# Kernel tuning notes

Hardware: AMD Instinct MI355X
Metric: run time of the kernel (lower is better)

## Reference

```python
import jax, jax.numpy as jnp
import numpy as np

N_ATOM, N_BOND, N_MOL, D = 250000, 250000, 10000, 64
BN_EPS = 1e-5


def _bn(x, gamma, beta):
    # torch BatchNorm1d training-mode math (biased variance)
    m = jnp.mean(x, axis=0)
    v = jnp.var(x, axis=0)
    return (x - m) * jax.lax.rsqrt(v + BN_EPS) * gamma + beta


def setup_inputs() -> dict:
    key = jax.random.key(0)
    ks = jax.random.split(key, 12)
    h = jax.random.normal(ks[0], (N_ATOM, D), jnp.float32)
    e = jax.random.normal(ks[1], (N_BOND, D), jnp.float32)
    u = jax.random.normal(ks[2], (N_MOL, D), jnp.float32)
    norm_atom = jax.random.uniform(ks[3], (N_ATOM, 1), jnp.float32)
    norm_bond = jax.random.uniform(ks[4], (N_BOND, 1), jnp.float32)
    bond_u = jax.random.randint(ks[5], (N_BOND,), 0, N_ATOM, jnp.int32)
    bond_v = jax.random.randint(ks[6], (N_BOND,), 0, N_ATOM, jnp.int32)
    atom2mol = jax.random.randint(ks[7], (N_ATOM,), 0, N_MOL, jnp.int32)
    bond2mol = jax.random.randint(ks[8], (N_BOND,), 0, N_MOL, jnp.int32)
    # 9 Linear layers A..I stacked: order A,B,C,D,E,F,G,H,I
    Ws = jax.random.normal(ks[9], (9, D, D), jnp.float32) * 0.05
    bs = jax.random.normal(ks[10], (9, D), jnp.float32) * 0.05
    bn_gamma = jnp.ones((3, D), jnp.float32)   # [e, h, u]
    bn_beta = jnp.zeros((3, D), jnp.float32)
    return dict(h=h, e=e, u=u, norm_atom=norm_atom, norm_bond=norm_bond,
                Ws=Ws, bs=bs, bn_gamma=bn_gamma, bn_beta=bn_beta,
                bond_u=bond_u, bond_v=bond_v, atom2mol=atom2mol, bond2mol=bond2mol)


def reference(h, e, u, norm_atom, norm_bond, Ws, bs, bn_gamma, bn_beta,
              bond_u, bond_v, atom2mol, bond2mol):
    lin = lambda x, i: x @ Ws[i] + bs[i]
    Ah, Dh, Eh = lin(h, 0), lin(h, 3), lin(h, 4)
    Be = lin(e, 1)
    Cu, Fu = lin(u, 2), lin(u, 5)

    # bond update: a2b (sum of Ah of both endpoints) + b2b self-loop + g2b broadcast
    e_new = Ah[bond_u] + Ah[bond_v] + Be + Cu[bond2mol]
    e_new = e_new * norm_bond                  # graph_norm
    e_new = _bn(e_new, bn_gamma[0], bn_beta[0])
    e_new = jax.nn.elu(e_new)

    # atom update: a2a self-loop + gated b2a (select_not_equal == other endpoint's Eh) + g2a
    sig = jax.nn.sigmoid(e_new)                # [N_BOND, D]
    dst = jnp.concatenate([bond_u, bond_v])    # each bond sends to both endpoints
    Eh_other = jnp.concatenate([Eh[bond_v], Eh[bond_u]])
    sig2 = jnp.concatenate([sig, sig])
    num = jax.ops.segment_sum(sig2 * Eh_other, dst, num_segments=N_ATOM)
    den = jax.ops.segment_sum(sig2, dst, num_segments=N_ATOM) + 1e-6
    h_new = Dh + num / den + Fu[atom2mol]
    h_new = h_new * norm_atom                  # graph_norm
    h_new = _bn(h_new, bn_gamma[1], bn_beta[1])
    h_new = jax.nn.elu(h_new)

    # global update: mean(Gh over atoms) + mean(He over bonds) + g2g self-loop Iu
    Gh, He, Iu = lin(h_new, 6), lin(e_new, 7), lin(u, 8)
    cnt_a = jax.ops.segment_sum(jnp.ones((N_ATOM, 1), h.dtype), atom2mol, num_segments=N_MOL)
    cnt_b = jax.ops.segment_sum(jnp.ones((N_BOND, 1), e.dtype), bond2mol, num_segments=N_MOL)
    u_new = (jax.ops.segment_sum(Gh, atom2mol, num_segments=N_MOL) / jnp.maximum(cnt_a, 1.0)
             + jax.ops.segment_sum(He, bond2mol, num_segments=N_MOL) / jnp.maximum(cnt_b, 1.0)
             + Iu)
    u_new = _bn(u_new, bn_gamma[2], bn_beta[2])
    u_new = jax.nn.elu(u_new)

    return h_new, e_new, u_new
```

## Files before the change

kernel.cpp:

```cpp
#include <hip/hip_runtime.h>
#include <cmath>

#define DD 64
#define TILE 64
#define BLK 256
#define NSLOT 64

__device__ __forceinline__ float elu_f(float x) {
  return x > 0.f ? x : expm1f(x);
}
__device__ __forceinline__ float sigmoid_fast(float x) {
  return __builtin_amdgcn_rcpf(1.f + __expf(-x));
}

__device__ __forceinline__ void fma4(float4& a, float s, const float4 b) {
  a.x = fmaf(s, b.x, a.x);
  a.y = fmaf(s, b.y, a.y);
  a.z = fmaf(s, b.z, a.z);
  a.w = fmaf(s, b.w, a.w);
}
__device__ __forceinline__ void add4(float4& a, const float4 b) {
  a.x += b.x; a.y += b.y; a.z += b.z; a.w += b.w;
}
__device__ __forceinline__ void sqacc4(float4& a, const float4 b) {
  a.x = fmaf(b.x, b.x, a.x);
  a.y = fmaf(b.y, b.y, a.y);
  a.z = fmaf(b.z, b.z, a.z);
  a.w = fmaf(b.w, b.w, a.w);
}
__device__ __forceinline__ void scale4(float4& a, float s) {
  a.x *= s; a.y *= s; a.z *= s; a.w *= s;
}

__device__ __forceinline__ void matmul_tile(const float (*xs)[DD + 4], const float (*wl)[DD],
                                            int r0, int c0, float4 acc[4]) {
#pragma unroll 2
  for (int k0 = 0; k0 < DD; k0 += 4) {
    float4 x0 = *(const float4*)&xs[r0 + 0][k0];
    float4 x1 = *(const float4*)&xs[r0 + 1][k0];
    float4 x2 = *(const float4*)&xs[r0 + 2][k0];
    float4 x3 = *(const float4*)&xs[r0 + 3][k0];
    float4 w0 = *(const float4*)&wl[k0 + 0][c0];
    float4 w1 = *(const float4*)&wl[k0 + 1][c0];
    float4 w2 = *(const float4*)&wl[k0 + 2][c0];
    float4 w3 = *(const float4*)&wl[k0 + 3][c0];
    fma4(acc[0], x0.x, w0); fma4(acc[0], x0.y, w1); fma4(acc[0], x0.z, w2); fma4(acc[0], x0.w, w3);
    fma4(acc[1], x1.x, w0); fma4(acc[1], x1.y, w1); fma4(acc[1], x1.z, w2); fma4(acc[1], x1.w, w3);
    fma4(acc[2], x2.x, w0); fma4(acc[2], x2.y, w1); fma4(acc[2], x2.z, w2); fma4(acc[2], x2.w, w3);
    fma4(acc[3], x3.x, w0); fma4(acc[3], x3.y, w1); fma4(acc[3], x3.z, w2); fma4(acc[3], x3.w, w3);
  }
}

__global__ void cnt_kernel(const int* __restrict__ a2m, int na,
                           const int* __restrict__ b2m, int nb,
                           const int* __restrict__ bu, const int* __restrict__ bv,
                           int* __restrict__ cnta_i, int* __restrict__ cntb_i,
                           int* __restrict__ deg) {
  int i = blockIdx.x * blockDim.x + threadIdx.x;
  if (i < na) {
    atomicAdd(&cnta_i[a2m[i]], 1);
  } else if (i < na + nb) {
    int b = i - na;
    atomicAdd(&cntb_i[b2m[b]], 1);
    atomicAdd(&deg[bu[b]], 1);
    atomicAdd(&deg[bv[b]], 1);
  }
}

__global__ void seg_alloc_kernel(const int* __restrict__ deg, int n,
                                 int* __restrict__ start, int* __restrict__ gcount) {
  int i = blockIdx.x * blockDim.x + threadIdx.x;
  int lane = threadIdx.x & 63;
  int d = (i < n) ? deg[i] : 0;
  int pre = d;
#pragma unroll
  for (int off = 1; off < 64; off <<= 1) {
    int t = __shfl_up(pre, off, 64);
    if (lane >= off) pre += t;
  }
  int total = __shfl(pre, 63, 64);
  int excl = pre - d;
  int base = 0;
  if (lane == 63) base = atomicAdd(gcount, total);
  base = __shfl(base, 63, 64);
  if (i < n) start[i] = base + excl;
}

__global__ void fill_kernel(const int* __restrict__ bu, const int* __restrict__ bv, int nb,
                            const int* __restrict__ start, int* __restrict__ cur,
                            int2* __restrict__ adj) {
  int b = blockIdx.x * blockDim.x + threadIdx.x;
  if (b < nb) {
    int a0 = bu[b], a1 = bv[b];
    int p = start[a0] + atomicAdd(&cur[a0], 1);
    adj[p] = make_int2(b, a1);
    int q = start[a1] + atomicAdd(&cur[a1], 1);
    adj[q] = make_int2(b, a0);
  }
}

__global__ void fill_mol_kernel(const int* __restrict__ a2m, int na,
                                const int* __restrict__ b2m, int nb,
                                const int* __restrict__ start_ma, int* __restrict__ cur_ma,
                                int* __restrict__ lista,
                                const int* __restrict__ start_mb, int* __restrict__ cur_mb,
                                int* __restrict__ listb) {
  int i = blockIdx.x * blockDim.x + threadIdx.x;
  if (i < na) {
    int m = a2m[i];
    lista[start_ma[m] + atomicAdd(&cur_ma[m], 1)] = i;
  } else if (i < na + nb) {
    int b = i - na;
    int m = b2m[b];
    listb[start_mb[m] + atomicAdd(&cur_mb[m], 1)] = b;
  }
}

__global__ __launch_bounds__(BLK) void lin2_kernel(
    const float* __restrict__ x, int nrows,
    const float* __restrict__ W0, const float* __restrict__ b0, float* __restrict__ out0,
    const float* __restrict__ W1, const float* __restrict__ b1, float* __restrict__ out1) {
  __shared__ __align__(16) float xs[TILE][DD + 4];
  __shared__ __align__(16) float w0[DD][DD];
  __shared__ __align__(16) float w1[DD][DD];
  const int tid = threadIdx.x;
  const int base = blockIdx.x * TILE;
  int rows = nrows - base; if (rows > TILE) rows = TILE;
  for (int l = tid; l < DD * DD; l += BLK) {
    int r = l >> 6, c = l & 63;
    xs[r][c] = (r < rows) ? x[(size_t)(base + r) * DD + c] : 0.f;
    w0[r][c] = W0[l];
    w1[r][c] = W1[l];
  }
  __syncthreads();
  const int tr = tid >> 4, tc = tid & 15;
  const int r0 = tr * 4, c0 = tc * 4;
  float4 accA[4], accB[4];
#pragma unroll
  for (int i = 0; i < 4; ++i) {
    accA[i] = make_float4(0.f, 0.f, 0.f, 0.f);
    accB[i] = make_float4(0.f, 0.f, 0.f, 0.f);
  }
#pragma unroll 1
  for (int k0 = 0; k0 < DD; k0 += 4) {
    float4 x0 = *(const float4*)&xs[r0 + 0][k0];
    float4 x1 = *(const float4*)&xs[r0 + 1][k0];
    float4 x2 = *(const float4*)&xs[r0 + 2][k0];
    float4 x3 = *(const float4*)&xs[r0 + 3][k0];
    float4 wa0 = *(const float4*)&w0[k0 + 0][c0];
    float4 wa1 = *(const float4*)&w0[k0 + 1][c0];
    float4 wa2 = *(const float4*)&w0[k0 + 2][c0];
    float4 wa3 = *(const float4*)&w0[k0 + 3][c0];
    float4 wb0 = *(const float4*)&w1[k0 + 0][c0];
    float4 wb1 = *(const float4*)&w1[k0 + 1][c0];
    float4 wb2 = *(const float4*)&w1[k0 + 2][c0];
    float4 wb3 = *(const float4*)&w1[k0 + 3][c0];
    fma4(accA[0], x0.x, wa0); fma4(accA[0], x0.y, wa1); fma4(accA[0], x0.z, wa2); fma4(accA[0], x0.w, wa3);
    fma4(accA[1], x1.x, wa0); fma4(accA[1], x1.y, wa1); fma4(accA[1], x1.z, wa2); fma4(accA[1], x1.w, wa3);
    fma4(accA[2], x2.x, wa0); fma4(accA[2], x2.y, wa1); fma4(accA[2], x2.z, wa2); fma4(accA[2], x2.w, wa3);
    fma4(accA[3], x3.x, wa0); fma4(accA[3], x3.y, wa1); fma4(accA[3], x3.z, wa2); fma4(accA[3], x3.w, wa3);
    fma4(accB[0], x0.x, wb0); fma4(accB[0], x0.y, wb1); fma4(accB[0], x0.z, wb2); fma4(accB[0], x0.w, wb3);
    fma4(accB[1], x1.x, wb0); fma4(accB[1], x1.y, wb1); fma4(accB[1], x1.z, wb2); fma4(accB[1], x1.w, wb3);
    fma4(accB[2], x2.x, wb0); fma4(accB[2], x2.y, wb1); fma4(accB[2], x2.z, wb2); fma4(accB[2], x2.w, wb3);
    fma4(accB[3], x3.x, wb0); fma4(accB[3], x3.y, wb1); fma4(accB[3], x3.z, wb2); fma4(accB[3], x3.w, wb3);
  }
  float4 bv0 = *(const float4*)&b0[c0];
  float4 bv1 = *(const float4*)&b1[c0];
#pragma unroll
  for (int i = 0; i < 4; ++i) {
    if (r0 + i < rows) {
      size_t rb = (size_t)(base + r0 + i) * DD + c0;
      float4 o0 = accA[i]; add4(o0, bv0);
      float4 o1 = accB[i]; add4(o1, bv1);
      *(float4*)&out0[rb] = o0;
      *(float4*)&out1[rb] = o1;
    }
  }
}

__global__ __launch_bounds__(BLK) void lin1_kernel(
    const float* __restrict__ x, int nrows,
    const float* __restrict__ W, const float* __restrict__ b, float* __restrict__ out) {
  __shared__ __align__(16) float xs[TILE][DD + 4];
  __shared__ __align__(16) float wl[DD][DD];
  const int tid = threadIdx.x;
  const int base = blockIdx.x * TILE;
  int rows = nrows - base; if (rows > TILE) rows = TILE;
  for (int l = tid; l < DD * DD; l += BLK) {
    int r = l >> 6, c = l & 63;
    xs[r][c] = (r < rows) ? x[(size_t)(base + r) * DD + c] : 0.f;
    wl[r][c] = W[l];
  }
  __syncthreads();
  const int tr = tid >> 4, tc = tid & 15;
  const int r0 = tr * 4, c0 = tc * 4;
  float4 acc[4];
#pragma unroll
  for (int i = 0; i < 4; ++i) acc[i] = make_float4(0.f, 0.f, 0.f, 0.f);
  matmul_tile(xs, wl, r0, c0, acc);
  float4 bv = *(const float4*)&b[c0];
#pragma unroll
  for (int i = 0; i < 4; ++i) {
    if (r0 + i < rows) {
      size_t rb = (size_t)(base + r0 + i) * DD + c0;
      float4 o = acc[i]; add4(o, bv);
      *(float4*)&out[rb] = o;
    }
  }
}

__global__ __launch_bounds__(BLK) void bond1_kernel(
    const float* __restrict__ e, int nrows, int ntiles,
    const float* __restrict__ W1, const float* __restrict__ b1,
    const float* __restrict__ Ah, const float* __restrict__ Cu,
    const int* __restrict__ bu, const int* __restrict__ bv, const int* __restrict__ b2m,
    const float* __restrict__ nrm,
    float* __restrict__ e_pre,
    float* __restrict__ psum, float* __restrict__ psq) {
  __shared__ __align__(16) float xs[TILE][DD + 4];
  __shared__ __align__(16) float wl[DD][DD];
  __shared__ int sbu[TILE], sbv[TILE], sbm[TILE];
  __shared__ float snb[TILE];
  __shared__ __align__(16) float red[16][DD];
  const int tid = threadIdx.x;
  const int tr = tid >> 4, tc = tid & 15, r0 = tr * 4, c0 = tc * 4;
  for (int l = tid; l < DD * DD; l += BLK) wl[l >> 6][l & 63] = W1[l];
  float4 bp = *(const float4*)&b1[c0];
  float4 lsum = make_float4(0.f, 0.f, 0.f, 0.f);
  float4 lsq  = make_float4(0.f, 0.f, 0.f, 0.f);
  for (int tile = blockIdx.x; tile < ntiles; tile += gridDim.x) {
    const int base = tile * TILE;
    int rows = nrows - base; if (rows > TILE) rows = TILE;
    __syncthreads();
    for (int l = tid; l < TILE * DD; l += BLK) {
      int r = l >> 6, c = l & 63;
      xs[r][c] = (r < rows) ? e[(size_t)(base + r) * DD + c] : 0.f;
    }
    if (tid < TILE) {
      bool v = tid < rows;
      int rb = base + tid;
      sbu[tid] = v ? bu[rb] : 0;
      sbv[tid] = v ? bv[rb] : 0;
      sbm[tid] = v ? b2m[rb] : 0;
      snb[tid] = v ? nrm[rb] : 0.f;
    }
    __syncthreads();
    float4 acc[4];
#pragma unroll
    for (int i = 0; i < 4; ++i) acc[i] = make_float4(0.f, 0.f, 0.f, 0.f);
    matmul_tile(xs, wl, r0, c0, acc);
#pragma unroll
    for (int i = 0; i < 4; ++i) {
      int r = r0 + i;
      if (r < rows) {
        int rb = base + r;
        float nb = snb[r];
        float4 ga = *(const float4*)&Ah[(size_t)sbu[r] * DD + c0];
        float4 gb = *(const float4*)&Ah[(size_t)sbv[r] * DD + c0];
        float4 gc = *(const float4*)&Cu[(size_t)sbm[r] * DD + c0];
        float4 o = acc[i];
        add4(o, bp); add4(o, ga); add4(o, gb); add4(o, gc);
        scale4(o, nb);
        add4(lsum, o); sqacc4(lsq, o);
        *(float4*)&e_pre[(size_t)rb * DD + c0] = o;
      }
    }
  }
  __syncthreads();
  *(float4*)&red[tr][c0] = lsum;
  __syncthreads();
  const int slot = (blockIdx.x & (NSLOT - 1)) * DD;
  if (tid < DD) {
    float s = 0.f;
#pragma unroll
    for (int t = 0; t < 16; ++t) s += red[t][tid];
    atomicAdd(&psum[slot + tid], s);
  }
  __syncthreads();
  *(float4*)&red[tr][c0] = lsq;
  __syncthreads();
  if (tid < DD) {
    float s = 0.f;
#pragma unroll
    for (int t = 0; t < 16; ++t) s += red[t][tid];
    atomicAdd(&psq[slot + tid], s);
  }
}

__global__ void bnfinal_kernel(const float* __restrict__ ssum, const float* __restrict__ ssq,
                               const float* __restrict__ gamma, const float* __restrict__ beta,
                               float invN, float* __restrict__ scale, float* __restrict__ shift) {
  int j = threadIdx.x;
  float m = ssum[j] * invN;
  float v = ssq[j] * invN - m * m;
  float sc = gamma[j] * rsqrtf(v + 1e-5f);
  scale[j] = sc;
  shift[j] = beta[j] - m * sc;
}

__global__ void bnfinal_slots_kernel(const float* __restrict__ psum, const float* __restrict__ psq,
                                     const float* __restrict__ gamma, const float* __restrict__ beta,
                                     float invN, float* __restrict__ scale, float* __restrict__ shift) {
  int j = threadIdx.x;
  float s = 0.f, q = 0.f;
#pragma unroll 8
  for (int t = 0; t < NSLOT; ++t) {
    s += psum[t * DD + j];
    q += psq[t * DD + j];
  }
  float m = s * invN;
  float v = q * invN - m * m;
  float sc = gamma[j] * rsqrtf(v + 1e-5f);
  scale[j] = sc;
  shift[j] = beta[j] - m * sc;
}

__global__ void bn_elu_vec_kernel(float* __restrict__ x, long n4,
                                  const float* __restrict__ scale,
                                  const float* __restrict__ shift) {
  long stride = (long)gridDim.x * blockDim.x;
  for (long i = blockIdx.x * (long)blockDim.x + threadIdx.x; i < n4; i += stride) {
    float4 v = ((float4*)x)[i];
    int c0 = (int)((i & 15) << 2);
    float4 sc = *(const float4*)&scale[c0];
    float4 sh = *(const float4*)&shift[c0];
    v.x = elu_f(fmaf(v.x, sc.x, sh.x));
    v.y = elu_f(fmaf(v.y, sc.y, sh.y));
    v.z = elu_f(fmaf(v.z, sc.z, sh.z));
    v.w = elu_f(fmaf(v.w, sc.w, sh.w));
    ((float4*)x)[i] = v;
  }
}

__global__ __launch_bounds__(BLK) void agg_fused_kernel(
    const float* __restrict__ e_act, const float* __restrict__ Eh,
    const float* __restrict__ Dhb, const float* __restrict__ Fu,
    const int* __restrict__ a2m, const float* __restrict__ nrm,
    const int* __restrict__ start, const int* __restrict__ deg,
    const int2* __restrict__ adj, int na,
    float* __restrict__ hpre,
    float* __restrict__ psum, float* __restrict__ psq) {
  const int tid = threadIdx.x;
  const int lane = tid & 63;
  const int wv = tid >> 6;
  const int wid = blockIdx.x * (BLK >> 6) + wv;
  float lsum = 0.f, lsq = 0.f;
  if (wid < na) {
    float dh = Dhb[(size_t)wid * DD + lane];
    float fu = Fu[(size_t)a2m[wid] * DD + lane];
    float nr = nrm[wid];
    int s = start[wid], d = deg[wid];
    float num = 0.f, den = 0.f;
    int k = 0;
    for (; k + 2 <= d; k += 2) {
      int2 e0 = adj[s + k];
      int2 e1 = adj[s + k + 1];
      float ev0 = e_act[(size_t)e0.x * DD + lane];
      float eh0 = Eh[(size_t)e0.y * DD + lane];
      float ev1 = e_act[(size_t)e1.x * DD + lane];
      float eh1 = Eh[(size_t)e1.y * DD + lane];
      float sg0 = sigmoid_fast(ev0);
      float sg1 = sigmoid_fast(ev1);
      num = fmaf(sg0, eh0, num); den += sg0;
      num = fmaf(sg1, eh1, num); den += sg1;
    }
    if (k < d) {
      int2 e0 = adj[s + k];
      float ev = e_act[(size_t)e0.x * DD + lane];
      float eh = Eh[(size_t)e0.y * DD + lane];
      float sg = sigmoid_fast(ev);
      num = fmaf(sg, eh, num); den += sg;
    }
    float o = (dh + num / (den + 1e-6f) + fu) * nr;
    hpre[(size_t)wid * DD + lane] = o;
    lsum = o;
    lsq = o * o;
  }
  __shared__ __align__(16) float red[BLK / 64][DD];
  red[wv][lane] = lsum;
  __syncthreads();
  if (tid < DD) {
    float s4 = red[0][tid] + red[1][tid] + red[2][tid] + red[3][tid];
    atomicAdd(&psum[(blockIdx.x & (NSLOT - 1)) * DD + tid], s4);
  }
  __syncthreads();
  red[wv][lane] = lsq;
  __syncthreads();
  if (tid < DD) {
    float s4 = red[0][tid] + red[1][tid] + red[2][tid] + red[3][tid];
    atomicAdd(&psq[(blockIdx.x & (NSLOT - 1)) * DD + tid], s4);
  }
}

__global__ __launch_bounds__(BLK) void molsum2_kernel(
    const float* __restrict__ srcA, const int* __restrict__ start_ma,
    const int* __restrict__ cnta, const int* __restrict__ lista,
    const float* __restrict__ srcB, const int* __restrict__ start_mb,
    const int* __restrict__ cntb, const int* __restrict__ listb,
    int nm, float* __restrict__ msa, float* __restrict__ msb) {
  int wid = (int)((blockIdx.x * (unsigned)blockDim.x + threadIdx.x) >> 6);
  int lane = threadIdx.x & 63;
  if (wid >= 2 * nm) return;
  const float* src;
  const int* list;
  float* out;
  int m, s, c;
  if (wid < nm) {
    m = wid; src = srcA; list = lista; out = msa;
    s = start_ma[m]; c = cnta[m];
  } else {
    m = wid - nm; src = srcB; list = listb; out = msb;
    s = start_mb[m]; c = cntb[m];
  }
  float acc = 0.f;
  int k = 0;
  for (; k + 2 <= c; k += 2) {
    int i0 = list[s + k], i1 = list[s + k + 1];
    float v0 = src[(size_t)i0 * DD + lane];
    float v1 = src[(size_t)i1 * DD + lane];
    acc += v0 + v1;
  }
  if (k < c) acc += src[(size_t)list[s + k] * DD + lane];
  out[(size_t)m * DD + lane] = acc;
}

__global__ __launch_bounds__(BLK) void global1_kernel(
    const float* __restrict__ u, int nrows,
    const float* __restrict__ W6, const float* __restrict__ W7, const float* __restrict__ W8,
    const float* __restrict__ b6, const float* __restrict__ b7, const float* __restrict__ b8,
    const float* __restrict__ msa, const float* __restrict__ msb,
    const int* __restrict__ cnta, const int* __restrict__ cntb,
    float* __restrict__ upre,
    float* __restrict__ ssum, float* __restrict__ ssq) {
  __shared__ __align__(16) float xsu[TILE][DD + 4];
  __shared__ __align__(16) float xsa[TILE][DD + 4];
  __shared__ __align__(16) float xsb[TILE][DD + 4];
  __shared__ __align__(16) float w6s[DD][DD];
  __shared__ __align__(16) float w7s[DD][DD];
  __shared__ __align__(16) float w8s[DD][DD];
  __shared__ float sfa[TILE], sfb[TILE];
  __shared__ __align__(16) float red[16][DD];
  const int tid = threadIdx.x;
  const int base = blockIdx.x * TILE;
  int rows = nrows - base; if (rows > TILE) rows = TILE;
  for (int l = tid; l < DD * DD; l += BLK) {
    int r = l >> 6, c = l & 63;
    w6s[r][c] = W6[l];
    w7s[r][c] = W7[l];
    w8s[r][c] = W8[l];
  }
  for (int l = tid; l < TILE * DD; l += BLK) {
    int r = l >> 6, c = l & 63;
    bool v = r < rows;
    float ca = 1.f, cb = 1.f;
    if (v) {
      int ia = cnta[base + r], ib = cntb[base + r];
      ca = ia > 0 ? (float)ia : 1.f;
      cb = ib > 0 ? (float)ib : 1.f;
    }
    xsu[r][c] = v ? u[(size_t)(base + r) * DD + c] : 0.f;
    xsa[r][c] = v ? msa[(size_t)(base + r) * DD + c] / ca : 0.f;
    xsb[r][c] = v ? msb[(size_t)(base + r) * DD + c] / cb : 0.f;
  }
  if (tid < TILE) {
    bool v = tid < rows;
    sfa[tid] = (v && cnta[base + tid] > 0) ? 1.f : 0.f;
    sfb[tid] = (v && cntb[base + tid] > 0) ? 1.f : 0.f;
  }
  __syncthreads();
  const int tr = tid >> 4, tc = tid & 15, r0 = tr * 4, c0 = tc * 4;
  float4 acc[4];
#pragma unroll
  for (int i = 0; i < 4; ++i) acc[i] = make_float4(0.f, 0.f, 0.f, 0.f);
  matmul_tile(xsu, w8s, r0, c0, acc);
  matmul_tile(xsa, w6s, r0, c0, acc);
  matmul_tile(xsb, w7s, r0, c0, acc);
  float4 b6v = *(const float4*)&b6[c0];
  float4 b7v = *(const float4*)&b7[c0];
  float4 b8v = *(const float4*)&b8[c0];
  float4 lsum = make_float4(0.f, 0.f, 0.f, 0.f);
  float4 lsq  = make_float4(0.f, 0.f, 0.f, 0.f);
#pragma unroll
  for (int i = 0; i < 4; ++i) {
    int r = r0 + i;
    if (r < rows) {
      size_t rb = (size_t)(base + r) * DD + c0;
      float fa = sfa[r], fb = sfb[r];
      float4 o = acc[i];
      o.x += b8v.x + fa * b6v.x + fb * b7v.x;
      o.y += b8v.y + fa * b6v.y + fb * b7v.y;
      o.z += b8v.z + fa * b6v.z + fb * b7v.z;
      o.w += b8v.w + fa * b6v.w + fb * b7v.w;
      add4(lsum, o); sqacc4(lsq, o);
      *(float4*)&upre[rb] = o;
    }
  }
  __syncthreads();
  *(float4*)&red[tr][c0] = lsum;
  __syncthreads();
  if (tid < DD) {
    float s = 0.f;
#pragma unroll
    for (int t = 0; t < 16; ++t) s += red[t][tid];
    atomicAdd(&ssum[tid], s);
  }
  __syncthreads();
  *(float4*)&red[tr][c0] = lsq;
  __syncthreads();
  if (tid < DD) {
    float s = 0.f;
#pragma unroll
    for (int t = 0; t < 16; ++t) s += red[t][tid];
    atomicAdd(&ssq[tid], s);
  }
}

extern "C" void kernel_launch(void* const* d_in, const int* in_sizes, int n_in,
                              void* d_out, int out_size, void* d_ws, size_t ws_size,
                              hipStream_t stream) {
  const float* h         = (const float*)d_in[0];
  const float* e         = (const float*)d_in[1];
  const float* u         = (const float*)d_in[2];
  const float* norm_atom = (const float*)d_in[3];
  const float* norm_bond = (const float*)d_in[4];
  const float* Ws        = (const float*)d_in[5];
  const float* bsarr     = (const float*)d_in[6];
  const float* bn_gamma  = (const float*)d_in[7];
  const float* bn_beta   = (const float*)d_in[8];
  const int* bond_u      = (const int*)d_in[9];
  const int* bond_v      = (const int*)d_in[10];
  const int* a2m         = (const int*)d_in[11];
  const int* b2m         = (const int*)d_in[12];

  const int NA = in_sizes[0] / DD;
  const int NB = in_sizes[1] / DD;
  const int NM = in_sizes[2] / DD;

  float* out_h = (float*)d_out;
  float* out_e = out_h + (size_t)NA * DD;
  float* out_u = out_e + (size_t)NB * DD;

  float* f     = (float*)d_ws;
  float* Ah    = f;
  float* Dhb   = Ah;
  float* Eh    = Ah + (size_t)NA * DD;
  float* Cu    = Eh + (size_t)NA * DD;
  float* Fu    = Cu + (size_t)NM * DD;
  float* msa   = Fu + (size_t)NM * DD;
  float* msb   = msa + (size_t)NM * DD;
  float* stats = msb + (size_t)NM * DD;
  float* sum_u = stats, *sq_u = stats + 64;
  float* psum_h = stats + 256;
  float* psq_h  = psum_h + NSLOT * DD;
  float* psum_e = psq_h + NSLOT * DD;
  float* psq_e  = psum_e + NSLOT * DD;
  int* deg     = (int*)(psq_e + NSLOT * DD);
  int* cur     = deg + NA;
  int* cnta_i  = cur + NA;
  int* cntb_i  = cnta_i + NM;
  int* cur_ma  = cntb_i + NM;
  int* cur_mb  = cur_ma + NM;
  int* gcounts = cur_mb + NM;
  float* bnp   = (float*)(gcounts + 4);
  float* sc_e = bnp, *sh_e = bnp + 64;
  float* sc_h = bnp + 128, *sh_h = bnp + 192;
  float* sc_u = bnp + 256, *sh_u = bnp + 320;
  int* start    = (int*)(bnp + 384);
  int* start_ma = start + NA;
  int* start_mb = start_ma + NM;
  int* lista    = start_mb + NM;
  int* listb    = lista + NA;
  int2* adj     = (int2*)(listb + NB);

  const float* W0 = Ws + 0 * 4096; const float* b0 = bsarr + 0 * 64;
  const float* W1 = Ws + 1 * 4096; const float* b1 = bsarr + 1 * 64;
  const float* W2 = Ws + 2 * 4096; const float* b2 = bsarr + 2 * 64;
  const float* W3 = Ws + 3 * 4096; const float* b3 = bsarr + 3 * 64;
  const float* W4 = Ws + 4 * 4096; const float* b4 = bsarr + 4 * 64;
  const float* W5 = Ws + 5 * 4096; const float* b5 = bsarr + 5 * 64;
  const float* W6 = Ws + 6 * 4096; const float* b6 = bsarr + 6 * 64;
  const float* W7 = Ws + 7 * 4096; const float* b7 = bsarr + 7 * 64;
  const float* W8 = Ws + 8 * 4096; const float* b8 = bsarr + 8 * 64;

  const int tiles_a = (NA + TILE - 1) / TILE;
  const int tiles_b = (NB + TILE - 1) / TILE;
  const int tiles_m = (NM + TILE - 1) / TILE;

  size_t zbytes = (256 + (size_t)NSLOT * DD * 4) * sizeof(float)
                + ((size_t)NA * 2 + (size_t)NM * 4 + 4) * sizeof(int);
  hipMemsetAsync(stats, 0, zbytes, stream);

  cnt_kernel<<<(NA + NB + BLK - 1) / BLK, BLK, 0, stream>>>(a2m, NA, b2m, NB,
                                                            bond_u, bond_v,
                                                            cnta_i, cntb_i, deg);
  seg_alloc_kernel<<<(NA + BLK - 1) / BLK, BLK, 0, stream>>>(deg, NA, start, gcounts + 0);
  seg_alloc_kernel<<<(NM + BLK - 1) / BLK, BLK, 0, stream>>>(cnta_i, NM, start_ma, gcounts + 1);
  seg_alloc_kernel<<<(NM + BLK - 1) / BLK, BLK, 0, stream>>>(cntb_i, NM, start_mb, gcounts + 2);
  fill_kernel<<<(NB + BLK - 1) / BLK, BLK, 0, stream>>>(bond_u, bond_v, NB, start, cur, adj);
  fill_mol_kernel<<<(NA + NB + BLK - 1) / BLK, BLK, 0, stream>>>(a2m, NA, b2m, NB,
                                                                 start_ma, cur_ma, lista,
                                                                 start_mb, cur_mb, listb);

  lin2_kernel<<<tiles_a, BLK, 0, stream>>>(h, NA, W0, b0, Ah, W4, b4, Eh);
  lin2_kernel<<<tiles_m, BLK, 0, stream>>>(u, NM, W2, b2, Cu, W5, b5, Fu);

  int nblk_b = tiles_b < 2048 ? tiles_b : 2048;
  bond1_kernel<<<nblk_b, BLK, 0, stream>>>(e, NB, tiles_b, W1, b1, Ah, Cu,
                                           bond_u, bond_v, b2m, norm_bond,
                                           out_e, psum_e, psq_e);
  bnfinal_slots_kernel<<<1, 64, 0, stream>>>(psum_e, psq_e, bn_gamma + 0, bn_beta + 0,
                                             1.f / (float)NB, sc_e, sh_e);

  {
    long n4 = (long)NB * (DD / 4);
    int blocks = (int)((n4 + BLK - 1) / BLK); if (blocks > 2048) blocks = 2048;
    bn_elu_vec_kernel<<<blocks, BLK, 0, stream>>>(out_e, n4, sc_e, sh_e);
  }

  lin1_kernel<<<tiles_a, BLK, 0, stream>>>(h, NA, W3, b3, Dhb);

  agg_fused_kernel<<<(NA + 3) / 4, BLK, 0, stream>>>(out_e, Eh, Dhb, Fu, a2m, norm_atom,
                                                     start, deg, adj, NA,
                                                     out_h, psum_h, psq_h);
  bnfinal_slots_kernel<<<1, 64, 0, stream>>>(psum_h, psq_h, bn_gamma + 64, bn_beta + 64,
                                             1.f / (float)NA, sc_h, sh_h);

  {
    long n4 = (long)NA * (DD / 4);
    int blocks = (int)((n4 + BLK - 1) / BLK); if (blocks > 2048) blocks = 2048;
    bn_elu_vec_kernel<<<blocks, BLK, 0, stream>>>(out_h, n4, sc_h, sh_h);
  }

  molsum2_kernel<<<(2 * NM + 3) / 4, BLK, 0, stream>>>(out_h, start_ma, cnta_i, lista,
                                                       out_e, start_mb, cntb_i, listb,
                                                       NM, msa, msb);

  global1_kernel<<<tiles_m, BLK, 0, stream>>>(u, NM, W6, W7, W8, b6, b7, b8,
                                              msa, msb, cnta_i, cntb_i,
                                              out_u, sum_u, sq_u);
  bnfinal_kernel<<<1, 64, 0, stream>>>(sum_u, sq_u, bn_gamma + 128, bn_beta + 128,
                                       1.f / (float)NM, sc_u, sh_u);
  {
    long n4 = (long)NM * (DD / 4);
    int blocks = (int)((n4 + BLK - 1) / BLK); if (blocks > 2048) blocks = 2048;
    bn_elu_vec_kernel<<<blocks, BLK, 0, stream>>>(out_u, n4, sc_u, sh_u);
  }
}
```

Measured before the change: 654.3 us.

## Fuse BN+ELU into gather consumers and fold Dh linear into aggregation

Removes the two standalone BN+ELU passes over the bond and atom arrays. The bond normalization is now applied on the fly when the aggregation gathers bond rows, and the molecule-sum kernel applies BN+ELU to each row and writes it back while accumulating. The separate Dh linear kernel is also dropped: each aggregation block loads W3 into shared memory and computes the per-atom dot products itself. The aim is to save full read/write passes over the two 64 MB tensors and one launch. The cost is redundant BN/ELU work on every bond gather, a 16KB W3 load per 4-atom block, and reliance on every row appearing exactly once in the mol lists for the write-back.

```diff
diff --git a/kernel.cpp b/kernel.cpp
--- a/kernel.cpp
+++ b/kernel.cpp
@@ -174,37 +174,6 @@
       float4 o1 = accB[i]; add4(o1, bv1);
       *(float4*)&out0[rb] = o0;
       *(float4*)&out1[rb] = o1;
-    }
-  }
-}
-
-__global__ __launch_bounds__(BLK) void lin1_kernel(
-    const float* __restrict__ x, int nrows,
-    const float* __restrict__ W, const float* __restrict__ b, float* __restrict__ out) {
-  __shared__ __align__(16) float xs[TILE][DD + 4];
-  __shared__ __align__(16) float wl[DD][DD];
-  const int tid = threadIdx.x;
-  const int base = blockIdx.x * TILE;
-  int rows = nrows - base; if (rows > TILE) rows = TILE;
-  for (int l = tid; l < DD * DD; l += BLK) {
-    int r = l >> 6, c = l & 63;
-    xs[r][c] = (r < rows) ? x[(size_t)(base + r) * DD + c] : 0.f;
-    wl[r][c] = W[l];
-  }
-  __syncthreads();
-  const int tr = tid >> 4, tc = tid & 15;
-  const int r0 = tr * 4, c0 = tc * 4;
-  float4 acc[4];
-#pragma unroll
-  for (int i = 0; i < 4; ++i) acc[i] = make_float4(0.f, 0.f, 0.f, 0.f);
-  matmul_tile(xs, wl, r0, c0, acc);
-  float4 bv = *(const float4*)&b[c0];
-#pragma unroll
-  for (int i = 0; i < 4; ++i) {
-    if (r0 + i < rows) {
-      size_t rb = (size_t)(base + r0 + i) * DD + c0;
-      float4 o = acc[i]; add4(o, bv);
-      *(float4*)&out[rb] = o;
     }
   }
 }
@@ -333,50 +302,68 @@
 }
 
 __global__ __launch_bounds__(BLK) void agg_fused_kernel(
-    const float* __restrict__ e_act, const float* __restrict__ Eh,
-    const float* __restrict__ Dhb, const float* __restrict__ Fu,
+    const float* __restrict__ h, const float* __restrict__ W3, const float* __restrict__ b3,
+    const float* __restrict__ e_pre, const float* __restrict__ Eh,
+    const float* __restrict__ Fu,
     const int* __restrict__ a2m, const float* __restrict__ nrm,
+    const float* __restrict__ sc_e, const float* __restrict__ sh_e,
     const int* __restrict__ start, const int* __restrict__ deg,
     const int2* __restrict__ adj, int na,
     float* __restrict__ hpre,
     float* __restrict__ psum, float* __restrict__ psq) {
+  __shared__ __align__(16) float w3s[DD][DD];
+  __shared__ __align__(16) float shh[BLK / 64][DD];
+  __shared__ __align__(16) float red[BLK / 64][DD];
   const int tid = threadIdx.x;
   const int lane = tid & 63;
   const int wv = tid >> 6;
   const int wid = blockIdx.x * (BLK >> 6) + wv;
+  for (int l = tid; l < DD * DD; l += BLK) w3s[l >> 6][l & 63] = W3[l];
+  __syncthreads();
   float lsum = 0.f, lsq = 0.f;
   if (wid < na) {
-    float dh = Dhb[(size_t)wid * DD + lane];
+    float hval = h[(size_t)wid * DD + lane];
     float fu = Fu[(size_t)a2m[wid] * DD + lane];
     float nr = nrm[wid];
+    float sce = sc_e[lane], she = sh_e[lane];
     int s = start[wid], d = deg[wid];
+    shh[wv][lane] = hval;
     float num = 0.f, den = 0.f;
     int k = 0;
     for (; k + 2 <= d; k += 2) {
       int2 e0 = adj[s + k];
       int2 e1 = adj[s + k + 1];
-      float ev0 = e_act[(size_t)e0.x * DD + lane];
+      float ep0 = e_pre[(size_t)e0.x * DD + lane];
       float eh0 = Eh[(size_t)e0.y * DD + lane];
-      float ev1 = e_act[(size_t)e1.x * DD + lane];
+      float ep1 = e_pre[(size_t)e1.x * DD + lane];
       float eh1 = Eh[(size_t)e1.y * DD + lane];
-      float sg0 = sigmoid_fast(ev0);
-      float sg1 = sigmoid_fast(ev1);
+      float sg0 = sigmoid_fast(elu_f(fmaf(ep0, sce, she)));
+      float sg1 = sigmoid_fast(elu_f(fmaf(ep1, sce, she)));
       num = fmaf(sg0, eh0, num); den += sg0;
       num = fmaf(sg1, eh1, num); den += sg1;
     }
     if (k < d) {
       int2 e0 = adj[s + k];
-      float ev = e_act[(size_t)e0.x * DD + lane];
+      float ep = e_pre[(size_t)e0.x * DD + lane];
       float eh = Eh[(size_t)e0.y * DD + lane];
-      float sg = sigmoid_fast(ev);
+      float sg = sigmoid_fast(elu_f(fmaf(ep, sce, she)));
       num = fmaf(sg, eh, num); den += sg;
+    }
+    float dh = b3[lane];
+#pragma unroll
+    for (int k0 = 0; k0 < DD; k0 += 4) {
+      float4 hv = *(const float4*)&shh[wv][k0];
+      dh = fmaf(hv.x, w3s[k0 + 0][lane], dh);
+      dh = fmaf(hv.y, w3s[k0 + 1][lane], dh);
+      dh = fmaf(hv.z, w3s[k0 + 2][lane], dh);
+      dh = fmaf(hv.w, w3s[k0 + 3][lane], dh);
     }
     float o = (dh + num / (den + 1e-6f) + fu) * nr;
     hpre[(size_t)wid * DD + lane] = o;
     lsum = o;
     lsq = o * o;
   }
-  __shared__ __align__(16) float red[BLK / 64][DD];
+  __syncthreads();
   red[wv][lane] = lsum;
   __syncthreads();
   if (tid < DD) {
@@ -393,34 +380,49 @@
 }
 
 __global__ __launch_bounds__(BLK) void molsum2_kernel(
-    const float* __restrict__ srcA, const int* __restrict__ start_ma,
+    float* __restrict__ rowsA, const int* __restrict__ start_ma,
     const int* __restrict__ cnta, const int* __restrict__ lista,
-    const float* __restrict__ srcB, const int* __restrict__ start_mb,
+    const float* __restrict__ scA, const float* __restrict__ shA,
+    float* __restrict__ rowsB, const int* __restrict__ start_mb,
     const int* __restrict__ cntb, const int* __restrict__ listb,
+    const float* __restrict__ scB, const float* __restrict__ shB,
     int nm, float* __restrict__ msa, float* __restrict__ msb) {
   int wid = (int)((blockIdx.x * (unsigned)blockDim.x + threadIdx.x) >> 6);
   int lane = threadIdx.x & 63;
   if (wid >= 2 * nm) return;
-  const float* src;
+  float* rows;
   const int* list;
   float* out;
+  float sc, sh;
   int m, s, c;
   if (wid < nm) {
-    m = wid; src = srcA; list = lista; out = msa;
+    m = wid; rows = rowsA; list = lista; out = msa;
     s = start_ma[m]; c = cnta[m];
+    sc = scA[lane]; sh = shA[lane];
   } else {
-    m = wid - nm; src = srcB; list = listb; out = msb;
+    m = wid - nm; rows = rowsB; list = listb; out = msb;
     s = start_mb[m]; c = cntb[m];
+    sc = scB[lane]; sh = shB[lane];
   }
   float acc = 0.f;
   int k = 0;
   for (; k + 2 <= c; k += 2) {
-    int i0 = list[s + k], i1 = list[s + k + 1];
-    float v0 = src[(size_t)i0 * DD + lane];
-    float v1 = src[(size_t)i1 * DD + lane];
-    acc += v0 + v1;
-  }
-  if (k < c) acc += src[(size_t)list[s + k] * DD + lane];
+    size_t i0 = (size_t)list[s + k] * DD + lane;
+    size_t i1 = (size_t)list[s + k + 1] * DD + lane;
+    float v0 = rows[i0];
+    float v1 = rows[i1];
+    float t0 = elu_f(fmaf(v0, sc, sh));
+    float t1 = elu_f(fmaf(v1, sc, sh));
+    rows[i0] = t0;
+    rows[i1] = t1;
+    acc += t0 + t1;
+  }
+  if (k < c) {
+    size_t i0 = (size_t)list[s + k] * DD + lane;
+    float t0 = elu_f(fmaf(rows[i0], sc, sh));
+    rows[i0] = t0;
+    acc += t0;
+  }
   out[(size_t)m * DD + lane] = acc;
 }
 
@@ -542,7 +544,6 @@
 
   float* f     = (float*)d_ws;
   float* Ah    = f;
-  float* Dhb   = Ah;
   float* Eh    = Ah + (size_t)NA * DD;
   float* Cu    = Eh + (size_t)NA * DD;
   float* Fu    = Cu + (size_t)NM * DD;
@@ -611,28 +612,16 @@
   bnfinal_slots_kernel<<<1, 64, 0, stream>>>(psum_e, psq_e, bn_gamma + 0, bn_beta + 0,
                                              1.f / (float)NB, sc_e, sh_e);
 
-  {
-    long n4 = (long)NB * (DD / 4);
-    int blocks = (int)((n4 + BLK - 1) / BLK); if (blocks > 2048) blocks = 2048;
-    bn_elu_vec_kernel<<<blocks, BLK, 0, stream>>>(out_e, n4, sc_e, sh_e);
-  }
-
-  lin1_kernel<<<tiles_a, BLK, 0, stream>>>(h, NA, W3, b3, Dhb);
-
-  agg_fused_kernel<<<(NA + 3) / 4, BLK, 0, stream>>>(out_e, Eh, Dhb, Fu, a2m, norm_atom,
+  agg_fused_kernel<<<(NA + 3) / 4, BLK, 0, stream>>>(h, W3, b3,
+                                                     out_e, Eh, Fu, a2m, norm_atom,
+                                                     sc_e, sh_e,
                                                      start, deg, adj, NA,
                                                      out_h, psum_h, psq_h);
   bnfinal_slots_kernel<<<1, 64, 0, stream>>>(psum_h, psq_h, bn_gamma + 64, bn_beta + 64,
                                              1.f / (float)NA, sc_h, sh_h);
 
-  {
-    long n4 = (long)NA * (DD / 4);
-    int blocks = (int)((n4 + BLK - 1) / BLK); if (blocks > 2048) blocks = 2048;
-    bn_elu_vec_kernel<<<blocks, BLK, 0, stream>>>(out_h, n4, sc_h, sh_h);
-  }
-
-  molsum2_kernel<<<(2 * NM + 3) / 4, BLK, 0, stream>>>(out_h, start_ma, cnta_i, lista,
-                                                       out_e, start_mb, cntb_i, listb,
+  molsum2_kernel<<<(2 * NM + 3) / 4, BLK, 0, stream>>>(out_h, start_ma, cnta_i, lista, sc_h, sh_h,
+                                                       out_e, start_mb, cntb_i, listb, sc_e, sh_e,
                                                        NM, msa, msb);
 
   global1_kernel<<<tiles_m, BLK, 0, stream>>>(u, NM, W6, W7, W8, b6, b7, b8,
```

New measurement: 682.8 us. 1.04x slower.
